# Performance work log

Measured on AMD Instinct MI355X. Metric: run time of the kernel, lower is better.

The kernel has to match this reference:

```python
import jax, jax.numpy as jnp
import numpy as np

B, H, FEAT = 16384, 256, 256
GX, GY, SW = 70, 70, 2


def setup_inputs() -> dict:
    key = jax.random.key(0)
    ks = jax.random.split(key, 10)
    stdv = 1.0 / np.sqrt(H)
    feats = jax.random.normal(ks[0], (B, FEAT), dtype=jnp.float32)
    coords = jax.random.randint(ks[1], (B, 2), 0, 64).astype(jnp.float32)
    input_tensor = jnp.concatenate([feats, coords], axis=1)  # [B, FEAT+2]
    hidden = jax.random.normal(ks[2], (B, H), dtype=jnp.float32)
    u = lambda k, shp: jax.random.uniform(k, shp, jnp.float32, -stdv, stdv)
    return {
        "input_tensor": input_tensor,
        "hidden": hidden,
        "w_ih": u(ks[3], (4 * H, FEAT)),
        "b_ih": u(ks[4], (4 * H,)),
        "w_hh": u(ks[5], (4 * H, H)),
        "b_hh": u(ks[6], (4 * H,)),
        "w_out": u(ks[7], (H, 2 * H)),
        "b_out": u(ks[8], (H,)),
        "memory": jax.random.normal(ks[9], (GX, GY, H), dtype=jnp.float32) * 0.1,
    }


def reference(input_tensor, hidden, w_ih, b_ih, w_hh, b_hh, w_out, b_out, memory):
    feature = input_tensor[:, :-2]
    grid = input_tensor[:, -2:].astype(jnp.int32) + SW  # [B,2]

    gi = feature @ w_ih.T + b_ih  # [B,4H]
    gh = hidden @ w_hh.T + b_hh   # [B,4H]
    i_r, i_i, i_n, i_s = jnp.split(gi, 4, axis=1)
    h_r, h_i, h_n, h_s = jnp.split(gh, 4, axis=1)

    resetgate = jax.nn.sigmoid(i_r + h_r)
    updategate = jax.nn.sigmoid(i_i + h_i)
    spatialgate = jax.nn.sigmoid(i_s + h_s)
    newgate = jnp.tanh(i_n + resetgate * h_n)

    # gather (2*SW+1)^2 neighborhood per sample from spatial memory
    gx = jnp.clip(grid[:, 0], 0, GX - 1)
    gy = jnp.clip(grid[:, 1], 0, GY - 1)
    off = jnp.arange(-SW, SW + 1)  # [K]
    xi = jnp.clip(gx[:, None] + off[None, :], 0, GX - 1)  # [B,K]
    yi = jnp.clip(gy[:, None] + off[None, :], 0, GY - 1)  # [B,K]
    K = 2 * SW + 1
    x_flat = jnp.broadcast_to(xi[:, :, None], (xi.shape[0], K, K)).reshape(xi.shape[0], -1)
    y_flat = jnp.broadcast_to(yi[:, None, :], (yi.shape[0], K, K)).reshape(yi.shape[0], -1)
    context = memory[x_flat, y_flat]  # [B, K*K, H]

    # attention (query is detached in original)
    q = jax.lax.stop_gradient(newgate)  # [B,H]
    attn = jnp.einsum('bh,bkh->bk', q, context)  # [B, K*K]
    attn = jnp.where(attn == 0, -jnp.inf, attn)
    w = jax.nn.softmax(attn, axis=1)
    w = jnp.where(jnp.isnan(w), 0.0, w)
    mix = jnp.einsum('bk,bkh->bh', w, context)  # [B,H]
    combined = jnp.concatenate([mix, q], axis=1)  # [B,2H]
    atten_cs = jnp.tanh(combined @ w_out.T + b_out)  # [B,H]

    curr_state = newgate + spatialgate * atten_cs
    output = curr_state + updategate * (hidden - curr_state)
    return output
```

## Files before the change

### kernel.cpp

```cpp
#include <hip/hip_runtime.h>
#include <stdint.h>

#define B_N 16384
#define H_N 256
#define IN_W 258
#define GX_N 70
#define GY_N 70
#define SW_N 2
#define KK_N 25

typedef __bf16 bf16x8 __attribute__((ext_vector_type(8)));
typedef __bf16 bf16x4 __attribute__((ext_vector_type(4)));
typedef __bf16 bf16x2 __attribute__((ext_vector_type(2)));
typedef float f32x4 __attribute__((ext_vector_type(4)));

#define AS1 __attribute__((address_space(1)))
#define AS3 __attribute__((address_space(3)))

static __device__ __forceinline__ void gload16(const void* g, void* l) {
    __builtin_amdgcn_global_load_lds((const AS1 uint32_t*)g, (AS3 uint32_t*)l, 16, 0, 0);
}

#define E_AB   8388608ULL
#define E_WF   8912896ULL
#define E_WOUT 9043968ULL
#define E_COMB 9043968ULL
#define E_UGSG 17432576ULL

__global__ __launch_bounds__(256) void cast_kernel(
    const float* __restrict__ in_t, const float* __restrict__ hid,
    const float* __restrict__ wih, const float* __restrict__ whh,
    const float* __restrict__ wout, __bf16* __restrict__ dst)
{
    size_t g = (size_t)blockIdx.x * blockDim.x + threadIdx.x;
    size_t stride = (size_t)gridDim.x * blockDim.x;
    for (size_t e = g * 4; e < E_WOUT; e += stride * 4) {
        const float* src;
        if (e < E_AB) {
            size_t row = e >> 9;
            size_t c = e & 511;
            src = (c < 256) ? (in_t + row * IN_W + c) : (hid + row * 256 + (c - 256));
        } else if (e < E_WF) {
            size_t off = e - E_AB;
            size_t j = off >> 9;
            size_t k = off & 511;
            size_t c = j >> 8;
            size_t col = j & 255;
            size_t base = (c == 0) ? 0 : (c == 1) ? 256 : (c == 2) ? 768 : 512;
            const float* srcm = (k < 256) ? wih : whh;
            src = srcm + (base + col) * 256 + (k & 255);
        } else {
            src = wout + (e - E_WF);
        }
        bf16x4 o;
        o.x = (__bf16)src[0];
        o.y = (__bf16)src[1];
        o.z = (__bf16)src[2];
        o.w = (__bf16)src[3];
        *reinterpret_cast<bf16x4*>(dst + e) = o;
    }
}

__global__ __launch_bounds__(256, 3) void gates_gemm(
    const __bf16* __restrict__ AB, const __bf16* __restrict__ wfull,
    const float* __restrict__ b_ih, const float* __restrict__ b_hh,
    __bf16* __restrict__ comb, __bf16* __restrict__ ugsg)
{
    __shared__ __bf16 ldsA[4096], ldsB[4096];
    const int t = threadIdx.x;
    const int lane = t & 63, w = t >> 6;
    const int lr = lane & 15, seg = lane >> 4;
    const int rb = blockIdx.x * 128;
    const int h0 = blockIdx.y * 32;

    const int r_s = t & 127;
    const int s_lo = t >> 7;
    const __bf16* gA = AB + (size_t)(rb + r_s) * 512 + s_lo * 8;
    const int wr = ((r_s >> 5) << 8) + h0 + (r_s & 31);
    const __bf16* gB = wfull + (size_t)wr * 512 + s_lo * 8;
    __bf16* lA = ldsA + t * 8;
    __bf16* lB = ldsB + t * 8;

    f32x4 acc_s[3][2][2], acc_ni[2][2], acc_nh[2][2];
#pragma unroll
    for (int hh = 0; hh < 2; hh++)
#pragma unroll
        for (int rh = 0; rh < 2; rh++) {
#pragma unroll
            for (int c = 0; c < 3; c++) acc_s[c][hh][rh] = (f32x4){0.f, 0.f, 0.f, 0.f};
            acc_ni[hh][rh] = (f32x4){0.f, 0.f, 0.f, 0.f};
            acc_nh[hh][rh] = (f32x4){0.f, 0.f, 0.f, 0.f};
        }

#pragma unroll 1
    for (int half = 0; half < 2; half++) {
        for (int kt = half * 256; kt < half * 256 + 256; kt += 32) {
            gload16(gA + kt, lA);
            gload16(gA + kt + 16, lA + 2048);
            gload16(gB + kt, lB);
            gload16(gB + kt + 16, lB + 2048);
            __syncthreads();

            bf16x8 af[2];
#pragma unroll
            for (int rh = 0; rh < 2; rh++) {
                int tr = w * 32 + rh * 16 + lr;
                af[rh] = *reinterpret_cast<const bf16x8*>(ldsA + seg * 1024 + tr * 8);
            }
#pragma unroll
            for (int c = 0; c < 4; c++)
#pragma unroll
                for (int hh = 0; hh < 2; hh++) {
                    int br = c * 32 + hh * 16 + lr;
                    bf16x8 bb = *reinterpret_cast<const bf16x8*>(ldsB + seg * 1024 + br * 8);
#pragma unroll
                    for (int rh = 0; rh < 2; rh++) {
                        if (c < 3)
                            acc_s[c][hh][rh] = __builtin_amdgcn_mfma_f32_16x16x32_bf16(af[rh], bb, acc_s[c][hh][rh], 0, 0, 0);
                        else if (half == 0)
                            acc_ni[hh][rh] = __builtin_amdgcn_mfma_f32_16x16x32_bf16(af[rh], bb, acc_ni[hh][rh], 0, 0, 0);
                        else
                            acc_nh[hh][rh] = __builtin_amdgcn_mfma_f32_16x16x32_bf16(af[rh], bb, acc_nh[hh][rh], 0, 0, 0);
                    }
                }
            __syncthreads();
        }
    }

#pragma unroll
    for (int hh = 0; hh < 2; hh++) {
        int col = h0 + hh * 16 + lr;
        float br_ = b_ih[col] + b_hh[col];
        float bi_ = b_ih[col + 256] + b_hh[col + 256];
        float bs_ = b_ih[col + 768] + b_hh[col + 768];
        float bni = b_ih[col + 512];
        float bnh = b_hh[col + 512];
#pragma unroll
        for (int rh = 0; rh < 2; rh++) {
#pragma unroll
            for (int r = 0; r < 4; r++) {
                int row = rb + w * 32 + rh * 16 + seg * 4 + r;
                float sr = acc_s[0][hh][rh][r] + br_;
                float si = acc_s[1][hh][rh][r] + bi_;
                float ss = acc_s[2][hh][rh][r] + bs_;
                float ni = acc_ni[hh][rh][r] + bni;
                float nh = acc_nh[hh][rh][r] + bnh;
                float rg = 1.f / (1.f + __expf(-sr));
                float ug = 1.f / (1.f + __expf(-si));
                float sg = 1.f / (1.f + __expf(-ss));
                float ng = tanhf(ni + rg * nh);
                comb[(size_t)row * 512 + 256 + col] = (__bf16)ng;
                bf16x2 us;
                us.x = (__bf16)ug;
                us.y = (__bf16)sg;
                *reinterpret_cast<bf16x2*>(ugsg + ((size_t)row * 256 + col) * 2) = us;
            }
        }
    }
}

__global__ __launch_bounds__(256) void attn_kernel(
    const float* __restrict__ in_t, const float* __restrict__ memory,
    __bf16* __restrict__ comb)
{
    const int w = threadIdx.x >> 6;
    const int lane = threadIdx.x & 63;
    const int b = blockIdx.x * 4 + w;
    const float* row_in = in_t + (size_t)b * IN_W;
    int gx = (int)row_in[256] + SW_N;
    int gy = (int)row_in[257] + SW_N;
    gx = min(max(gx, 0), GX_N - 1);
    gy = min(max(gy, 0), GY_N - 1);

    bf16x4 qb = *reinterpret_cast<const bf16x4*>(comb + (size_t)b * 512 + 256 + lane * 4);
    float q0 = (float)qb.x, q1 = (float)qb.y, q2 = (float)qb.z, q3 = (float)qb.w;

    float m = -INFINITY, d = 0.f;
    float o0 = 0.f, o1 = 0.f, o2 = 0.f, o3 = 0.f;
#pragma unroll
    for (int k = 0; k < KK_N; k++) {
        int i = k / 5, j = k % 5;
        int xi = min(max(gx + i - SW_N, 0), GX_N - 1);
        int yj = min(max(gy + j - SW_N, 0), GY_N - 1);
        const f32x4* cp = reinterpret_cast<const f32x4*>(memory + ((size_t)xi * GY_N + yj) * H_N);
        f32x4 v = cp[lane];
        float p = q0 * v.x + q1 * v.y + q2 * v.z + q3 * v.w;
        for (int off = 32; off; off >>= 1) p += __shfl_xor(p, off, 64);
        float a = (p == 0.f) ? -INFINITY : p;
        float mn = fmaxf(m, a);
        if (mn != -INFINITY) {
            float alpha = __expf(m - mn);
            float e = __expf(a - mn);
            d = d * alpha + e;
            o0 = o0 * alpha + e * v.x;
            o1 = o1 * alpha + e * v.y;
            o2 = o2 * alpha + e * v.z;
            o3 = o3 * alpha + e * v.w;
            m = mn;
        }
    }
    float inv = (d != 0.f) ? 1.f / d : 0.f;
    bf16x4 ob;
    ob.x = (__bf16)(o0 * inv);
    ob.y = (__bf16)(o1 * inv);
    ob.z = (__bf16)(o2 * inv);
    ob.w = (__bf16)(o3 * inv);
    *reinterpret_cast<bf16x4*>(comb + (size_t)b * 512 + lane * 4) = ob;
}

__global__ __launch_bounds__(256, 4) void out_gemm(
    const __bf16* __restrict__ comb, const __bf16* __restrict__ woB,
    const float* __restrict__ b_out, const __bf16* __restrict__ ugsg,
    const float* __restrict__ hidden, float* __restrict__ out)
{
    __shared__ __bf16 ldsA[4096], ldsB[2048];
    const int t = threadIdx.x;
    const int lane = t & 63, w = t >> 6;
    const int lr = lane & 15, seg = lane >> 4;
    const int rb = blockIdx.x * 128;
    const int n0 = blockIdx.y * 64;

    const int rA = t & 127;
    const int sA = t >> 7;
    const __bf16* gA = comb + (size_t)(rb + rA) * 512 + sA * 8;
    __bf16* lA = ldsA + t * 8;
    const __bf16* gB = woB + (size_t)(n0 + (t & 63)) * 512 + (t >> 6) * 8;
    __bf16* lB = ldsB + t * 8;

    f32x4 acc[2][4];
#pragma unroll
    for (int rh = 0; rh < 2; rh++)
#pragma unroll
        for (int ct = 0; ct < 4; ct++) acc[rh][ct] = (f32x4){0.f, 0.f, 0.f, 0.f};

    for (int kt = 0; kt < 512; kt += 32) {
        gload16(gA + kt, lA);
        gload16(gA + kt + 16, lA + 2048);
        gload16(gB + kt, lB);
        __syncthreads();

        bf16x8 af[2];
#pragma unroll
        for (int rh = 0; rh < 2; rh++) {
            int tr = w * 32 + rh * 16 + lr;
            af[rh] = *reinterpret_cast<const bf16x8*>(ldsA + seg * 1024 + tr * 8);
        }
#pragma unroll
        for (int ct = 0; ct < 4; ct++) {
            bf16x8 bb = *reinterpret_cast<const bf16x8*>(ldsB + seg * 512 + (ct * 16 + lr) * 8);
#pragma unroll
            for (int rh = 0; rh < 2; rh++)
                acc[rh][ct] = __builtin_amdgcn_mfma_f32_16x16x32_bf16(af[rh], bb, acc[rh][ct], 0, 0, 0);
        }
        __syncthreads();
    }

#pragma unroll
    for (int ct = 0; ct < 4; ct++) {
        int col = n0 + ct * 16 + lr;
        float bo = b_out[col];
#pragma unroll
        for (int rh = 0; rh < 2; rh++) {
#pragma unroll
            for (int r = 0; r < 4; r++) {
                int row = rb + w * 32 + rh * 16 + seg * 4 + r;
                size_t idx = (size_t)row * 256 + col;
                float acs = tanhf(acc[rh][ct][r] + bo);
                float ng = (float)comb[(size_t)row * 512 + 256 + col];
                bf16x2 us = *reinterpret_cast<const bf16x2*>(ugsg + idx * 2);
                float ug = (float)us.x, sg = (float)us.y;
                float curr = ng + sg * acs;
                out[idx] = curr + ug * (hidden[idx] - curr);
            }
        }
    }
}

extern "C" void kernel_launch(void* const* d_in, const int* in_sizes, int n_in,
                              void* d_out, int out_size, void* d_ws, size_t ws_size,
                              hipStream_t stream) {
    const float* input_t = (const float*)d_in[0];
    const float* hidden  = (const float*)d_in[1];
    const float* w_ih    = (const float*)d_in[2];
    const float* b_ih    = (const float*)d_in[3];
    const float* w_hh    = (const float*)d_in[4];
    const float* b_hh    = (const float*)d_in[5];
    const float* w_out   = (const float*)d_in[6];
    const float* b_out   = (const float*)d_in[7];
    const float* memory  = (const float*)d_in[8];
    float* out = (float*)d_out;

    __bf16* base  = (__bf16*)d_ws;
    __bf16* AB    = base;
    __bf16* wfull = base + E_AB;
    __bf16* woutB = base + E_WF;
    __bf16* comb  = base + E_COMB;
    __bf16* ugsg  = base + E_UGSG;

    cast_kernel<<<4096, 256, 0, stream>>>(input_t, hidden, w_ih, w_hh, w_out, base);
    gates_gemm<<<dim3(128, 8), 256, 0, stream>>>(AB, wfull, b_ih, b_hh, comb, ugsg);
    attn_kernel<<<4096, 256, 0, stream>>>(input_t, memory, comb);
    out_gemm<<<dim3(128, 4), 256, 0, stream>>>(comb, woutB, b_out, ugsg, hidden, out);
}
```

Baseline: 209.5 us.

## Fuse all stages into one persistent cooperative kernel with grid syncs

Merges the cast, gates GEMM, attention and output GEMM kernels into a single cooperative persistent kernel that separates the stages with grid-wide syncs, so three separate kernel launches and their gaps disappear. The gates GEMM and out GEMM tiles are reordered for L2 locality, and the out GEMM tile shrinks from 128 to 64 rows, giving 1024 tiles. The costs are grid.sync overhead, occupancy-limited block counts sized by an occupancy query on every call, and a less efficient smaller out-GEMM tile.

```diff
diff --git a/kernel.cpp b/kernel.cpp
--- a/kernel.cpp
+++ b/kernel.cpp
@@ -1,5 +1,8 @@
 #include <hip/hip_runtime.h>
+#include <hip/hip_cooperative_groups.h>
 #include <stdint.h>
+
+namespace cg = cooperative_groups;
 
 #define B_N 16384
 #define H_N 256
@@ -27,250 +30,245 @@
 #define E_COMB 9043968ULL
 #define E_UGSG 17432576ULL
 
-__global__ __launch_bounds__(256) void cast_kernel(
+__global__ __launch_bounds__(256) void fused_kernel(
     const float* __restrict__ in_t, const float* __restrict__ hid,
-    const float* __restrict__ wih, const float* __restrict__ whh,
-    const float* __restrict__ wout, __bf16* __restrict__ dst)
+    const float* __restrict__ wih, const float* __restrict__ b_ih,
+    const float* __restrict__ whh, const float* __restrict__ b_hh,
+    const float* __restrict__ wout, const float* __restrict__ b_out,
+    const float* __restrict__ memory, float* __restrict__ out,
+    __bf16* __restrict__ base)
 {
-    size_t g = (size_t)blockIdx.x * blockDim.x + threadIdx.x;
-    size_t stride = (size_t)gridDim.x * blockDim.x;
-    for (size_t e = g * 4; e < E_WOUT; e += stride * 4) {
-        const float* src;
-        if (e < E_AB) {
-            size_t row = e >> 9;
-            size_t c = e & 511;
-            src = (c < 256) ? (in_t + row * IN_W + c) : (hid + row * 256 + (c - 256));
-        } else if (e < E_WF) {
-            size_t off = e - E_AB;
-            size_t j = off >> 9;
-            size_t k = off & 511;
-            size_t c = j >> 8;
-            size_t col = j & 255;
-            size_t base = (c == 0) ? 0 : (c == 1) ? 256 : (c == 2) ? 768 : 512;
-            const float* srcm = (k < 256) ? wih : whh;
-            src = srcm + (base + col) * 256 + (k & 255);
-        } else {
-            src = wout + (e - E_WF);
-        }
-        bf16x4 o;
-        o.x = (__bf16)src[0];
-        o.y = (__bf16)src[1];
-        o.z = (__bf16)src[2];
-        o.w = (__bf16)src[3];
-        *reinterpret_cast<bf16x4*>(dst + e) = o;
-    }
-}
-
-__global__ __launch_bounds__(256, 3) void gates_gemm(
-    const __bf16* __restrict__ AB, const __bf16* __restrict__ wfull,
-    const float* __restrict__ b_ih, const float* __restrict__ b_hh,
-    __bf16* __restrict__ comb, __bf16* __restrict__ ugsg)
-{
-    __shared__ __bf16 ldsA[4096], ldsB[4096];
+    __shared__ __bf16 smem[8192];
+    cg::grid_group grid = cg::this_grid();
+    const int nb = gridDim.x;
+    const int bid = blockIdx.x;
     const int t = threadIdx.x;
     const int lane = t & 63, w = t >> 6;
     const int lr = lane & 15, seg = lane >> 4;
-    const int rb = blockIdx.x * 128;
-    const int h0 = blockIdx.y * 32;
-
-    const int r_s = t & 127;
-    const int s_lo = t >> 7;
-    const __bf16* gA = AB + (size_t)(rb + r_s) * 512 + s_lo * 8;
-    const int wr = ((r_s >> 5) << 8) + h0 + (r_s & 31);
-    const __bf16* gB = wfull + (size_t)wr * 512 + s_lo * 8;
-    __bf16* lA = ldsA + t * 8;
-    __bf16* lB = ldsB + t * 8;
-
-    f32x4 acc_s[3][2][2], acc_ni[2][2], acc_nh[2][2];
-#pragma unroll
-    for (int hh = 0; hh < 2; hh++)
-#pragma unroll
-        for (int rh = 0; rh < 2; rh++) {
-#pragma unroll
-            for (int c = 0; c < 3; c++) acc_s[c][hh][rh] = (f32x4){0.f, 0.f, 0.f, 0.f};
-            acc_ni[hh][rh] = (f32x4){0.f, 0.f, 0.f, 0.f};
-            acc_nh[hh][rh] = (f32x4){0.f, 0.f, 0.f, 0.f};
-        }
+
+    __bf16* AB    = base;
+    __bf16* wfull = base + E_AB;
+    __bf16* woutB = base + E_WF;
+    __bf16* comb  = base + E_COMB;
+    __bf16* ugsg  = base + E_UGSG;
+
+    {
+        size_t g = (size_t)bid * 256 + t;
+        size_t stride = (size_t)nb * 256;
+        for (size_t e = g * 4; e < E_WOUT; e += stride * 4) {
+            const float* src;
+            if (e < E_AB) {
+                size_t row = e >> 9;
+                size_t c = e & 511;
+                src = (c < 256) ? (in_t + row * IN_W + c) : (hid + row * 256 + (c - 256));
+            } else if (e < E_WF) {
+                size_t off = e - E_AB;
+                size_t j = off >> 9;
+                size_t k = off & 511;
+                size_t c = j >> 8;
+                size_t col = j & 255;
+                size_t cb = (c == 0) ? 0 : (c == 1) ? 256 : (c == 2) ? 768 : 512;
+                const float* srcm = (k < 256) ? wih : whh;
+                src = srcm + (cb + col) * 256 + (k & 255);
+            } else {
+                src = wout + (e - E_WF);
+            }
+            bf16x4 o;
+            o.x = (__bf16)src[0];
+            o.y = (__bf16)src[1];
+            o.z = (__bf16)src[2];
+            o.w = (__bf16)src[3];
+            *reinterpret_cast<bf16x4*>(base + e) = o;
+        }
+    }
+    grid.sync();
+
+    for (int tile = bid; tile < 1024; tile += nb) {
+        int j = tile >> 3;
+        int rb = ((tile & 7) | ((j & 15) << 3)) << 7;
+        int h0 = (j >> 4) << 5;
+
+        __bf16* ldsA = smem;
+        __bf16* ldsB = smem + 4096;
+        const int r_s = t & 127;
+        const int s_lo = t >> 7;
+        const __bf16* gA = AB + (size_t)(rb + r_s) * 512 + s_lo * 8;
+        const int wr = ((r_s >> 5) << 8) + h0 + (r_s & 31);
+        const __bf16* gB = wfull + (size_t)wr * 512 + s_lo * 8;
+        __bf16* lA = ldsA + t * 8;
+        __bf16* lB = ldsB + t * 8;
+
+        f32x4 acc_s[3][2][2], acc_ni[2][2], acc_nh[2][2];
+#pragma unroll
+        for (int hh = 0; hh < 2; hh++)
+#pragma unroll
+            for (int rh = 0; rh < 2; rh++) {
+#pragma unroll
+                for (int c = 0; c < 3; c++) acc_s[c][hh][rh] = (f32x4){0.f, 0.f, 0.f, 0.f};
+                acc_ni[hh][rh] = (f32x4){0.f, 0.f, 0.f, 0.f};
+                acc_nh[hh][rh] = (f32x4){0.f, 0.f, 0.f, 0.f};
+            }
 
 #pragma unroll 1
-    for (int half = 0; half < 2; half++) {
-        for (int kt = half * 256; kt < half * 256 + 256; kt += 32) {
+        for (int half = 0; half < 2; half++) {
+            for (int kt = half * 256; kt < half * 256 + 256; kt += 32) {
+                gload16(gA + kt, lA);
+                gload16(gA + kt + 16, lA + 2048);
+                gload16(gB + kt, lB);
+                gload16(gB + kt + 16, lB + 2048);
+                __syncthreads();
+
+                bf16x8 af[2];
+#pragma unroll
+                for (int rh = 0; rh < 2; rh++) {
+                    int tr = w * 32 + rh * 16 + lr;
+                    af[rh] = *reinterpret_cast<const bf16x8*>(ldsA + seg * 1024 + tr * 8);
+                }
+#pragma unroll
+                for (int c = 0; c < 4; c++)
+#pragma unroll
+                    for (int hh = 0; hh < 2; hh++) {
+                        int br = c * 32 + hh * 16 + lr;
+                        bf16x8 bb = *reinterpret_cast<const bf16x8*>(ldsB + seg * 1024 + br * 8);
+#pragma unroll
+                        for (int rh = 0; rh < 2; rh++) {
+                            if (c < 3)
+                                acc_s[c][hh][rh] = __builtin_amdgcn_mfma_f32_16x16x32_bf16(af[rh], bb, acc_s[c][hh][rh], 0, 0, 0);
+                            else if (half == 0)
+                                acc_ni[hh][rh] = __builtin_amdgcn_mfma_f32_16x16x32_bf16(af[rh], bb, acc_ni[hh][rh], 0, 0, 0);
+                            else
+                                acc_nh[hh][rh] = __builtin_amdgcn_mfma_f32_16x16x32_bf16(af[rh], bb, acc_nh[hh][rh], 0, 0, 0);
+                        }
+                    }
+                __syncthreads();
+            }
+        }
+
+#pragma unroll
+        for (int hh = 0; hh < 2; hh++) {
+            int col = h0 + hh * 16 + lr;
+            float br_ = b_ih[col] + b_hh[col];
+            float bi_ = b_ih[col + 256] + b_hh[col + 256];
+            float bs_ = b_ih[col + 768] + b_hh[col + 768];
+            float bni = b_ih[col + 512];
+            float bnh = b_hh[col + 512];
+#pragma unroll
+            for (int rh = 0; rh < 2; rh++) {
+#pragma unroll
+                for (int r = 0; r < 4; r++) {
+                    int row = rb + w * 32 + rh * 16 + seg * 4 + r;
+                    float sr = acc_s[0][hh][rh][r] + br_;
+                    float si = acc_s[1][hh][rh][r] + bi_;
+                    float ss = acc_s[2][hh][rh][r] + bs_;
+                    float ni = acc_ni[hh][rh][r] + bni;
+                    float nh = acc_nh[hh][rh][r] + bnh;
+                    float rg = 1.f / (1.f + __expf(-sr));
+                    float ug = 1.f / (1.f + __expf(-si));
+                    float sg = 1.f / (1.f + __expf(-ss));
+                    float ng = tanhf(ni + rg * nh);
+                    comb[(size_t)row * 512 + 256 + col] = (__bf16)ng;
+                    bf16x2 us;
+                    us.x = (__bf16)ug;
+                    us.y = (__bf16)sg;
+                    *reinterpret_cast<bf16x2*>(ugsg + ((size_t)row * 256 + col) * 2) = us;
+                }
+            }
+        }
+    }
+    grid.sync();
+
+    for (int b0 = bid; b0 < 4096; b0 += nb) {
+        int b = b0 * 4 + w;
+        const float* row_in = in_t + (size_t)b * IN_W;
+        int gx = (int)row_in[256] + SW_N;
+        int gy = (int)row_in[257] + SW_N;
+        gx = min(max(gx, 0), GX_N - 1);
+        gy = min(max(gy, 0), GY_N - 1);
+
+        bf16x4 qb = *reinterpret_cast<const bf16x4*>(comb + (size_t)b * 512 + 256 + lane * 4);
+        float q0 = (float)qb.x, q1 = (float)qb.y, q2 = (float)qb.z, q3 = (float)qb.w;
+
+        float m = -INFINITY, d = 0.f;
+        float o0 = 0.f, o1 = 0.f, o2 = 0.f, o3 = 0.f;
+#pragma unroll
+        for (int k = 0; k < KK_N; k++) {
+            int i = k / 5, jj = k % 5;
+            int xi = min(max(gx + i - SW_N, 0), GX_N - 1);
+            int yj = min(max(gy + jj - SW_N, 0), GY_N - 1);
+            const f32x4* cp = reinterpret_cast<const f32x4*>(memory + ((size_t)xi * GY_N + yj) * H_N);
+            f32x4 v = cp[lane];
+            float p = q0 * v.x + q1 * v.y + q2 * v.z + q3 * v.w;
+            for (int off = 32; off; off >>= 1) p += __shfl_xor(p, off, 64);
+            float a = (p == 0.f) ? -INFINITY : p;
+            float mn = fmaxf(m, a);
+            if (mn != -INFINITY) {
+                float alpha = __expf(m - mn);
+                float e = __expf(a - mn);
+                d = d * alpha + e;
+                o0 = o0 * alpha + e * v.x;
+                o1 = o1 * alpha + e * v.y;
+                o2 = o2 * alpha + e * v.z;
+                o3 = o3 * alpha + e * v.w;
+                m = mn;
+            }
+        }
+        float inv = (d != 0.f) ? 1.f / d : 0.f;
+        bf16x4 ob;
+        ob.x = (__bf16)(o0 * inv);
+        ob.y = (__bf16)(o1 * inv);
+        ob.z = (__bf16)(o2 * inv);
+        ob.w = (__bf16)(o3 * inv);
+        *reinterpret_cast<bf16x4*>(comb + (size_t)b * 512 + lane * 4) = ob;
+    }
+    grid.sync();
+
+    for (int tile = bid; tile < 1024; tile += nb) {
+        int j = tile >> 3;
+        int rx = (tile & 7) | ((j & 31) << 3);
+        int cy = j >> 5;
+        int rb = rx << 6;
+        int n0 = cy << 6;
+
+        __bf16* ldsA = smem;
+        __bf16* ldsB = smem + 2048;
+        const __bf16* gA = comb + (size_t)(rb + (t & 63)) * 512 + (t >> 6) * 8;
+        const __bf16* gB = woutB + (size_t)(n0 + (t & 63)) * 512 + (t >> 6) * 8;
+        __bf16* lA = ldsA + t * 8;
+        __bf16* lB = ldsB + t * 8;
+
+        f32x4 acc[4];
+#pragma unroll
+        for (int ct = 0; ct < 4; ct++) acc[ct] = (f32x4){0.f, 0.f, 0.f, 0.f};
+
+        for (int kt = 0; kt < 512; kt += 32) {
             gload16(gA + kt, lA);
-            gload16(gA + kt + 16, lA + 2048);
             gload16(gB + kt, lB);
-            gload16(gB + kt + 16, lB + 2048);
             __syncthreads();
 
-            bf16x8 af[2];
-#pragma unroll
-            for (int rh = 0; rh < 2; rh++) {
-                int tr = w * 32 + rh * 16 + lr;
-                af[rh] = *reinterpret_cast<const bf16x8*>(ldsA + seg * 1024 + tr * 8);
-            }
-#pragma unroll
-            for (int c = 0; c < 4; c++)
-#pragma unroll
-                for (int hh = 0; hh < 2; hh++) {
-                    int br = c * 32 + hh * 16 + lr;
-                    bf16x8 bb = *reinterpret_cast<const bf16x8*>(ldsB + seg * 1024 + br * 8);
-#pragma unroll
-                    for (int rh = 0; rh < 2; rh++) {
-                        if (c < 3)
-                            acc_s[c][hh][rh] = __builtin_amdgcn_mfma_f32_16x16x32_bf16(af[rh], bb, acc_s[c][hh][rh], 0, 0, 0);
-                        else if (half == 0)
-                            acc_ni[hh][rh] = __builtin_amdgcn_mfma_f32_16x16x32_bf16(af[rh], bb, acc_ni[hh][rh], 0, 0, 0);
-                        else
-                            acc_nh[hh][rh] = __builtin_amdgcn_mfma_f32_16x16x32_bf16(af[rh], bb, acc_nh[hh][rh], 0, 0, 0);
-                    }
-                }
+            int tr = w * 16 + lr;
+            bf16x8 af = *reinterpret_cast<const bf16x8*>(ldsA + seg * 512 + tr * 8);
+#pragma unroll
+            for (int ct = 0; ct < 4; ct++) {
+                bf16x8 bb = *reinterpret_cast<const bf16x8*>(ldsB + seg * 512 + (ct * 16 + lr) * 8);
+                acc[ct] = __builtin_amdgcn_mfma_f32_16x16x32_bf16(af, bb, acc[ct], 0, 0, 0);
+            }
             __syncthreads();
         }
-    }
-
-#pragma unroll
-    for (int hh = 0; hh < 2; hh++) {
-        int col = h0 + hh * 16 + lr;
-        float br_ = b_ih[col] + b_hh[col];
-        float bi_ = b_ih[col + 256] + b_hh[col + 256];
-        float bs_ = b_ih[col + 768] + b_hh[col + 768];
-        float bni = b_ih[col + 512];
-        float bnh = b_hh[col + 512];
-#pragma unroll
-        for (int rh = 0; rh < 2; rh++) {
+
+#pragma unroll
+        for (int ct = 0; ct < 4; ct++) {
+            int col = n0 + ct * 16 + lr;
+            float bo = b_out[col];
 #pragma unroll
             for (int r = 0; r < 4; r++) {
-                int row = rb + w * 32 + rh * 16 + seg * 4 + r;
-                float sr = acc_s[0][hh][rh][r] + br_;
-                float si = acc_s[1][hh][rh][r] + bi_;
-                float ss = acc_s[2][hh][rh][r] + bs_;
-                float ni = acc_ni[hh][rh][r] + bni;
-                float nh = acc_nh[hh][rh][r] + bnh;
-                float rg = 1.f / (1.f + __expf(-sr));
-                float ug = 1.f / (1.f + __expf(-si));
-                float sg = 1.f / (1.f + __expf(-ss));
-                float ng = tanhf(ni + rg * nh);
-                comb[(size_t)row * 512 + 256 + col] = (__bf16)ng;
-                bf16x2 us;
-                us.x = (__bf16)ug;
-                us.y = (__bf16)sg;
-                *reinterpret_cast<bf16x2*>(ugsg + ((size_t)row * 256 + col) * 2) = us;
-            }
-        }
-    }
-}
-
-__global__ __launch_bounds__(256) void attn_kernel(
-    const float* __restrict__ in_t, const float* __restrict__ memory,
-    __bf16* __restrict__ comb)
-{
-    const int w = threadIdx.x >> 6;
-    const int lane = threadIdx.x & 63;
-    const int b = blockIdx.x * 4 + w;
-    const float* row_in = in_t + (size_t)b * IN_W;
-    int gx = (int)row_in[256] + SW_N;
-    int gy = (int)row_in[257] + SW_N;
-    gx = min(max(gx, 0), GX_N - 1);
-    gy = min(max(gy, 0), GY_N - 1);
-
-    bf16x4 qb = *reinterpret_cast<const bf16x4*>(comb + (size_t)b * 512 + 256 + lane * 4);
-    float q0 = (float)qb.x, q1 = (float)qb.y, q2 = (float)qb.z, q3 = (float)qb.w;
-
-    float m = -INFINITY, d = 0.f;
-    float o0 = 0.f, o1 = 0.f, o2 = 0.f, o3 = 0.f;
-#pragma unroll
-    for (int k = 0; k < KK_N; k++) {
-        int i = k / 5, j = k % 5;
-        int xi = min(max(gx + i - SW_N, 0), GX_N - 1);
-        int yj = min(max(gy + j - SW_N, 0), GY_N - 1);
-        const f32x4* cp = reinterpret_cast<const f32x4*>(memory + ((size_t)xi * GY_N + yj) * H_N);
-        f32x4 v = cp[lane];
-        float p = q0 * v.x + q1 * v.y + q2 * v.z + q3 * v.w;
-        for (int off = 32; off; off >>= 1) p += __shfl_xor(p, off, 64);
-        float a = (p == 0.f) ? -INFINITY : p;
-        float mn = fmaxf(m, a);
-        if (mn != -INFINITY) {
-            float alpha = __expf(m - mn);
-            float e = __expf(a - mn);
-            d = d * alpha + e;
-            o0 = o0 * alpha + e * v.x;
-            o1 = o1 * alpha + e * v.y;
-            o2 = o2 * alpha + e * v.z;
-            o3 = o3 * alpha + e * v.w;
-            m = mn;
-        }
-    }
-    float inv = (d != 0.f) ? 1.f / d : 0.f;
-    bf16x4 ob;
-    ob.x = (__bf16)(o0 * inv);
-    ob.y = (__bf16)(o1 * inv);
-    ob.z = (__bf16)(o2 * inv);
-    ob.w = (__bf16)(o3 * inv);
-    *reinterpret_cast<bf16x4*>(comb + (size_t)b * 512 + lane * 4) = ob;
-}
-
-__global__ __launch_bounds__(256, 4) void out_gemm(
-    const __bf16* __restrict__ comb, const __bf16* __restrict__ woB,
-    const float* __restrict__ b_out, const __bf16* __restrict__ ugsg,
-    const float* __restrict__ hidden, float* __restrict__ out)
-{
-    __shared__ __bf16 ldsA[4096], ldsB[2048];
-    const int t = threadIdx.x;
-    const int lane = t & 63, w = t >> 6;
-    const int lr = lane & 15, seg = lane >> 4;
-    const int rb = blockIdx.x * 128;
-    const int n0 = blockIdx.y * 64;
-
-    const int rA = t & 127;
-    const int sA = t >> 7;
-    const __bf16* gA = comb + (size_t)(rb + rA) * 512 + sA * 8;
-    __bf16* lA = ldsA + t * 8;
-    const __bf16* gB = woB + (size_t)(n0 + (t & 63)) * 512 + (t >> 6) * 8;
-    __bf16* lB = ldsB + t * 8;
-
-    f32x4 acc[2][4];
-#pragma unroll
-    for (int rh = 0; rh < 2; rh++)
-#pragma unroll
-        for (int ct = 0; ct < 4; ct++) acc[rh][ct] = (f32x4){0.f, 0.f, 0.f, 0.f};
-
-    for (int kt = 0; kt < 512; kt += 32) {
-        gload16(gA + kt, lA);
-        gload16(gA + kt + 16, lA + 2048);
-        gload16(gB + kt, lB);
-        __syncthreads();
-
-        bf16x8 af[2];
-#pragma unroll
-        for (int rh = 0; rh < 2; rh++) {
-            int tr = w * 32 + rh * 16 + lr;
-            af[rh] = *reinterpret_cast<const bf16x8*>(ldsA + seg * 1024 + tr * 8);
-        }
-#pragma unroll
-        for (int ct = 0; ct < 4; ct++) {
-            bf16x8 bb = *reinterpret_cast<const bf16x8*>(ldsB + seg * 512 + (ct * 16 + lr) * 8);
-#pragma unroll
-            for (int rh = 0; rh < 2; rh++)
-                acc[rh][ct] = __builtin_amdgcn_mfma_f32_16x16x32_bf16(af[rh], bb, acc[rh][ct], 0, 0, 0);
-        }
-        __syncthreads();
-    }
-
-#pragma unroll
-    for (int ct = 0; ct < 4; ct++) {
-        int col = n0 + ct * 16 + lr;
-        float bo = b_out[col];
-#pragma unroll
-        for (int rh = 0; rh < 2; rh++) {
-#pragma unroll
-            for (int r = 0; r < 4; r++) {
-                int row = rb + w * 32 + rh * 16 + seg * 4 + r;
+                int row = rb + w * 16 + seg * 4 + r;
                 size_t idx = (size_t)row * 256 + col;
-                float acs = tanhf(acc[rh][ct][r] + bo);
+                float acs = tanhf(acc[ct][r] + bo);
                 float ng = (float)comb[(size_t)row * 512 + 256 + col];
                 bf16x2 us = *reinterpret_cast<const bf16x2*>(ugsg + idx * 2);
                 float ug = (float)us.x, sg = (float)us.y;
                 float curr = ng + sg * acs;
-                out[idx] = curr + ug * (hidden[idx] - curr);
+                out[idx] = curr + ug * (hid[idx] - curr);
             }
         }
     }
@@ -289,16 +287,19 @@
     const float* b_out   = (const float*)d_in[7];
     const float* memory  = (const float*)d_in[8];
     float* out = (float*)d_out;
-
-    __bf16* base  = (__bf16*)d_ws;
-    __bf16* AB    = base;
-    __bf16* wfull = base + E_AB;
-    __bf16* woutB = base + E_WF;
-    __bf16* comb  = base + E_COMB;
-    __bf16* ugsg  = base + E_UGSG;
-
-    cast_kernel<<<4096, 256, 0, stream>>>(input_t, hidden, w_ih, w_hh, w_out, base);
-    gates_gemm<<<dim3(128, 8), 256, 0, stream>>>(AB, wfull, b_ih, b_hh, comb, ugsg);
-    attn_kernel<<<4096, 256, 0, stream>>>(input_t, memory, comb);
-    out_gemm<<<dim3(128, 4), 256, 0, stream>>>(comb, woutB, b_out, ugsg, hidden, out);
+    __bf16* base = (__bf16*)d_ws;
+
+    int occ = 0;
+    hipError_t oe = hipOccupancyMaxActiveBlocksPerMultiprocessor(&occ, fused_kernel, 256, 0);
+    if (oe != hipSuccess || occ < 1) occ = 1;
+    int nb = occ * 256;
+    if (nb > 1024) nb = 1024;
+
+    void* args[] = {
+        (void*)&input_t, (void*)&hidden, (void*)&w_ih, (void*)&b_ih,
+        (void*)&w_hh, (void*)&b_hh, (void*)&w_out, (void*)&b_out,
+        (void*)&memory, (void*)&out, (void*)&base
+    };
+    hipLaunchCooperativeKernel((const void*)fused_kernel, dim3(nb), dim3(256),
+                               args, 0, stream);
 }
```

New measurement: 533.0 us. 2.54x slower.
